# Kernel optimization log

Hardware: AMD Instinct MI355X
Metric: run time of the kernel (lower is better)

The kernel has to match this reference:

```python
import jax, jax.numpy as jnp
import numpy as np

NUM_ITERATIONS = 3


def _squash(s):
    # s: [B, J, S]. Faithful to the torch code: squash norm is computed over
    # dim=2 of s_j [B,1,J,S,1], i.e. the num_unit (J) axis here.
    mag_sq = jnp.sum(s * s, axis=1, keepdims=True)  # [B, 1, S]
    mag = jnp.sqrt(mag_sq)
    return s * (mag_sq / (1.0 + mag_sq) / mag)


def setup_inputs() -> dict:
    key = jax.random.key(0)
    k1, k2 = jax.random.split(key)
    B, U, C, J, S = 128, 8, 2048, 32, 16
    x = jax.random.normal(k1, (B, U, C), dtype=jnp.float32)
    W = jax.random.normal(k2, (1, C, J, S, U), dtype=jnp.float32)
    return {"x": x, "W": W}


def reference(x, W):
    # x: [B, in_unit, in_channel]; W: [1, C, J, S, U]
    xt = jnp.swapaxes(x, 1, 2)          # [B, C, U]
    Wc = W[0]                           # [C, J, S, U]
    # u_hat = W @ x (per input capsule c, output capsule j): [B, C, J, S]
    u_hat = jnp.einsum('cjsu,bcu->bcjs', Wc, xt)
    B, C, J, _ = u_hat.shape
    b = jnp.zeros((C, J), dtype=u_hat.dtype)
    v = None
    for _ in range(NUM_ITERATIONS):
        # legacy F.softmax on 4D [1,C,J,1] defaults to dim=1 -> over C
        c = jax.nn.softmax(b, axis=0)                      # [C, J]
        s = jnp.einsum('cj,bcjs->bjs', c, u_hat)           # [B, J, S]
        v = _squash(s)                                     # [B, J, S]
        # agreement, mean over batch (keepdim handled by shape [C,J])
        b = b + jnp.einsum('bcjs,bjs->cj', u_hat, v) / B
    return v[..., None]  # [B, num_unit, unit_size, 1] == v_j.squeeze(1)
```

## Files before the change

### kernel.cpp

```cpp
#include <hip/hip_runtime.h>
#include <hip/hip_bf16.h>

#define BB 128
#define UU 8
#define CC 2048
#define JJ 32
#define SS 16

typedef unsigned int u32;
typedef unsigned short u16;
typedef __attribute__((ext_vector_type(8))) short bf16x8;
typedef __attribute__((ext_vector_type(4))) float f32x4;

__device__ __forceinline__ float bflo(u32 p) { return __uint_as_float(p << 16); }
__device__ __forceinline__ float bfhi(u32 p) { return __uint_as_float(p & 0xffff0000u); }
__device__ __forceinline__ u32 f2b(float f) {
    u32 bits = __float_as_uint(f);
    u32 r = bits + 0x7fffu + ((bits >> 16) & 1u);
    return r >> 16;
}
__device__ __forceinline__ u32 pack2(float a, float b) { return f2b(a) | (f2b(b) << 16); }
__device__ __forceinline__ uint4 scale4(uint4 p, float cw) {
    uint4 o;
    o.x = pack2(bflo(p.x) * cw, bfhi(p.x) * cw);
    o.y = pack2(bflo(p.y) * cw, bfhi(p.y) * cw);
    o.z = pack2(bflo(p.z) * cw, bfhi(p.z) * cw);
    o.w = pack2(bflo(p.w) * cw, bfhi(p.w) * cw);
    return o;
}

__global__ __launch_bounds__(256) void k_prep(const float* __restrict__ x,
                                              const float* __restrict__ W,
                                              u16* __restrict__ xA,
                                              u16* __restrict__ xB,
                                              u16* __restrict__ Wn,
                                              float* __restrict__ bbp) {
    __shared__ uint4 ldsu[16][129];
    int blk = blockIdx.x, t = threadIdx.x;
    if (blk < 1024) {
        int b = blk >> 3;
        int c = (blk & 7) * 256 + t;
        const float* xf = x + (size_t)b * UU * CC;
        float v[8];
#pragma unroll
        for (int u = 0; u < 8; ++u) v[u] = xf[u * CC + c];
        uint4 p;
        p.x = pack2(v[0], v[1]);
        p.y = pack2(v[2], v[3]);
        p.z = pack2(v[4], v[5]);
        p.w = pack2(v[6], v[7]);
        ((uint4*)xA)[(size_t)b * CC + c] = p;
    } else if (blk < 2048) {
        int bb2 = blk - 1024;
        int u = bb2 >> 7, c0 = (bb2 & 127) * 16;
        float* ldsf = (float*)ldsu;
        int b = t >> 1, h = t & 1;
        const float4* x4 = (const float4*)(x + ((size_t)b * UU + u) * CC + c0);
        float4 lo = x4[h * 2], hi = x4[h * 2 + 1];
        ldsf[(h * 8 + 0) * 129 + b] = lo.x; ldsf[(h * 8 + 1) * 129 + b] = lo.y;
        ldsf[(h * 8 + 2) * 129 + b] = lo.z; ldsf[(h * 8 + 3) * 129 + b] = lo.w;
        ldsf[(h * 8 + 4) * 129 + b] = hi.x; ldsf[(h * 8 + 5) * 129 + b] = hi.y;
        ldsf[(h * 8 + 6) * 129 + b] = hi.z; ldsf[(h * 8 + 7) * 129 + b] = hi.w;
        __syncthreads();
        int ci = t >> 4, k8 = t & 15;
        const float* r = ldsf + ci * 129 + k8 * 8;
        uint4 p;
        p.x = pack2(r[0], r[1]);
        p.y = pack2(r[2], r[3]);
        p.z = pack2(r[4], r[5]);
        p.w = pack2(r[6], r[7]);
        ((uint4*)xB)[((size_t)u * CC + c0 + ci) * 16 + k8] = p;
    } else if (blk < 2560) {
        int bb2 = blk - 2048;
        int ct = bb2 & 127, nt = bb2 >> 7;
        int c0 = ct * 16, n0 = nt * 128;
        const float4* Wf = (const float4*)W;
        for (int q = t; q < 2048; q += 256) {
            int ci = q >> 7, ni = q & 127;
            size_t widx = (size_t)(c0 + ci) * 512 + n0 + ni;
            float4 lo = Wf[2 * widx], hi = Wf[2 * widx + 1];
            uint4 o;
            o.x = pack2(lo.x, lo.y);
            o.y = pack2(lo.z, lo.w);
            o.z = pack2(hi.x, hi.y);
            o.w = pack2(hi.z, hi.w);
            ldsu[ci][ni] = o;
        }
        __syncthreads();
        for (int q = t; q < 2048; q += 256) {
            int ni = q >> 4, ci = q & 15;
            ((uint4*)Wn)[(size_t)(n0 + ni) * 2048 + c0 + ci] = ldsu[ci][ni];
        }
    } else {
        int base = (blk - 2560) * 4096 + t;
#pragma unroll
        for (int r = 0; r < 16; ++r) bbp[base + r * 256] = 0.f;
    }
}

__global__ __launch_bounds__(256) void k_softmax(const float* __restrict__ bbp,
                                                 float* __restrict__ ccp) {
    int j = blockIdx.x, t = threadIdx.x;
    __shared__ float red[4];
    __shared__ float bcast[2];
    const float* row = bbp + j * CC;
    float m = -1e30f;
    for (int c = t; c < CC; c += 256) m = fmaxf(m, row[c]);
#pragma unroll
    for (int o = 32; o > 0; o >>= 1) m = fmaxf(m, __shfl_down(m, o, 64));
    if ((t & 63) == 0) red[t >> 6] = m;
    __syncthreads();
    if (t == 0) bcast[0] = fmaxf(fmaxf(red[0], red[1]), fmaxf(red[2], red[3]));
    __syncthreads();
    float mm = bcast[0];
    float ssum = 0.f;
    for (int c = t; c < CC; c += 256) ssum += expf(row[c] - mm);
#pragma unroll
    for (int o = 32; o > 0; o >>= 1) ssum += __shfl_down(ssum, o, 64);
    if ((t & 63) == 0) red[t >> 6] = ssum;
    __syncthreads();
    if (t == 0) bcast[1] = red[0] + red[1] + red[2] + red[3];
    __syncthreads();
    float inv = 1.0f / bcast[1];
    for (int c = t; c < CC; c += 256) ccp[j * CC + c] = expf(row[c] - mm) * inv;
}

__global__ __launch_bounds__(512) void k_gemmA(const u16* __restrict__ xA,
                                               const u16* __restrict__ Wn,
                                               const float* __restrict__ ccp,
                                               int use_cc,
                                               float* __restrict__ spart) {
    __shared__ uint4 As[128][9];
    __shared__ uint4 Bs[128][9];
    const uint4* xA4 = (const uint4*)xA;
    const uint4* Wn4 = (const uint4*)Wn;
    int t = threadIdx.x;
    int sl = blockIdx.x >> 2;
    int n0 = (blockIdx.x & 3) * 128;
    int w = t >> 6, lane = t & 63;
    int mh = w & 1, nq = w >> 1;
    int ln = lane & 15, quad = lane >> 4;
    f32x4 acc[4][2];
#pragma unroll
    for (int mt = 0; mt < 4; ++mt)
#pragma unroll
        for (int nt2 = 0; nt2 < 2; ++nt2) acc[mt][nt2] = {0.f, 0.f, 0.f, 0.f};

    for (int ch = 0; ch < 4; ++ch) {
        int cbase = sl * 32 + ch * 8;
#pragma unroll
        for (int r2 = 0; r2 < 2; ++r2) {
            int q = t + r2 * 512;
            int row = q >> 3, k8 = q & 7;
            As[row][k8] = xA4[(size_t)row * 2048 + cbase + k8];
        }
#pragma unroll
        for (int r2 = 0; r2 < 2; ++r2) {
            int q = t + r2 * 512;
            int ni = q >> 3, k8 = q & 7;
            uint4 wb = Wn4[(size_t)(n0 + ni) * 2048 + cbase + k8];
            if (use_cc) wb = scale4(wb, ccp[((n0 + ni) >> 4) * CC + cbase + k8]);
            Bs[ni][k8] = wb;
        }
        __syncthreads();
#pragma unroll
        for (int st = 0; st < 2; ++st) {
            bf16x8 af[4], bf[2];
#pragma unroll
            for (int mt = 0; mt < 4; ++mt)
                af[mt] = __builtin_bit_cast(bf16x8,
                         As[mh * 64 + mt * 16 + ln][st * 4 + quad]);
#pragma unroll
            for (int nt2 = 0; nt2 < 2; ++nt2)
                bf[nt2] = __builtin_bit_cast(bf16x8,
                          Bs[nq * 32 + nt2 * 16 + ln][st * 4 + quad]);
#pragma unroll
            for (int mt = 0; mt < 4; ++mt)
#pragma unroll
                for (int nt2 = 0; nt2 < 2; ++nt2)
                    acc[mt][nt2] = __builtin_amdgcn_mfma_f32_16x16x32_bf16(
                        af[mt], bf[nt2], acc[mt][nt2], 0, 0, 0);
        }
        __syncthreads();
    }
    float* outp = spart + sl * (BB * JJ * SS);
#pragma unroll
    for (int mt = 0; mt < 4; ++mt)
#pragma unroll
        for (int nt2 = 0; nt2 < 2; ++nt2)
#pragma unroll
            for (int r = 0; r < 4; ++r) {
                int b = mh * 64 + mt * 16 + quad * 4 + r;
                int n = n0 + nq * 32 + nt2 * 16 + ln;
                outp[b * 512 + n] = acc[mt][nt2][r];
            }
}

__global__ __launch_bounds__(512) void k_rsq(const float* __restrict__ spart,
                                             u16* __restrict__ vB,
                                             float* __restrict__ out,
                                             float scale_pre, int write_out) {
    __shared__ float s[512];
    __shared__ float sc[16];
    int b = blockIdx.x, n = threadIdx.x;
    float v = 0.f;
#pragma unroll
    for (int sl = 0; sl < 64; ++sl) v += spart[sl * (BB * JJ * SS) + b * 512 + n];
    v *= scale_pre;
    s[n] = v;
    __syncthreads();
    if (n < 16) {
        float msq = 0.f;
#pragma unroll
        for (int jj = 0; jj < 32; ++jj) {
            float tv = s[jj * 16 + n];
            msq = fmaf(tv, tv, msq);
        }
        sc[n] = msq / ((1.f + msq) * sqrtf(fmaxf(msq, 1e-30f)));
    }
    __syncthreads();
    float vv = s[n] * sc[n & 15];
    vB[n * BB + b] = (u16)f2b(vv);
    if (write_out) out[b * 512 + n] = vv;
}

__global__ __launch_bounds__(256) void k_gemmBf(const u16* __restrict__ vB,
                                                const u16* __restrict__ xB,
                                                const u16* __restrict__ Wn,
                                                float* __restrict__ bbp) {
    const bf16x8* A8 = (const bf16x8*)vB;
    const bf16x8* B8 = (const bf16x8*)xB;
    const uint4* Wn4 = (const uint4*)Wn;
    int t = threadIdx.x;
    int w = t >> 6, lane = t & 63;
    int gw = blockIdx.x * 4 + w;
    int u = gw >> 10, rest = gw & 1023;
    int nt = rest & 15, c0 = (rest >> 4) * 32;
    int n0 = nt * 32;
    int ln = lane & 15, quad = lane >> 4;
    bf16x8 av[2][4], bx[2][4];
#pragma unroll
    for (int mt = 0; mt < 2; ++mt)
#pragma unroll
        for (int st = 0; st < 4; ++st)
            av[mt][st] = A8[(n0 + mt * 16 + ln) * 16 + quad + 4 * st];
#pragma unroll
    for (int ct = 0; ct < 2; ++ct)
#pragma unroll
        for (int st = 0; st < 4; ++st)
            bx[ct][st] = B8[((size_t)u * CC + c0 + ct * 16 + ln) * 16 + quad + 4 * st];
    f32x4 acc[2][2];
    acc[0][0] = {0.f, 0.f, 0.f, 0.f};
    acc[0][1] = acc[0][0]; acc[1][0] = acc[0][0]; acc[1][1] = acc[0][0];
#pragma unroll
    for (int st = 0; st < 4; ++st)
#pragma unroll
        for (int mt = 0; mt < 2; ++mt)
#pragma unroll
            for (int ct = 0; ct < 2; ++ct)
                acc[mt][ct] = __builtin_amdgcn_mfma_f32_16x16x32_bf16(
                    av[mt][st], bx[ct][st], acc[mt][ct], 0, 0, 0);
#pragma unroll
    for (int mt = 0; mt < 2; ++mt) {
        int j = 2 * nt + mt;
#pragma unroll
        for (int ct = 0; ct < 2; ++ct) {
            int c = c0 + ct * 16 + ln;
            float val = 0.f;
#pragma unroll
            for (int r = 0; r < 4; ++r) {
                int n = n0 + mt * 16 + quad * 4 + r;
                uint4 wp = Wn4[(size_t)n * 2048 + c];
                u32 warr[4] = {wp.x, wp.y, wp.z, wp.w};
                u32 ww = warr[u >> 1];
                float wv = (u & 1) ? bfhi(ww) : bflo(ww);
                val = fmaf(acc[mt][ct][r], wv, val);
            }
            val += __shfl_xor(val, 16, 64);
            val += __shfl_xor(val, 32, 64);
            if (quad == 0)
                atomicAdd(&bbp[j * CC + c], val * (1.0f / BB));
        }
    }
}

extern "C" void kernel_launch(void* const* d_in, const int* in_sizes, int n_in,
                              void* d_out, int out_size, void* d_ws, size_t ws_size,
                              hipStream_t stream) {
    const float* x = (const float*)d_in[0];
    const float* W = (const float*)d_in[1];
    if (in_sizes[0] == CC * JJ * SS * UU) {
        x = (const float*)d_in[1];
        W = (const float*)d_in[0];
    }
    float* out = (float*)d_out;

    char* ws = (char*)d_ws;
    float* spart = (float*)ws;
    u16* xA = (u16*)(ws + (16u << 20));
    u16* xB = (u16*)(ws + (20u << 20));
    u16* Wn = (u16*)(ws + (24u << 20));
    size_t b48 = (size_t)48u << 20;
    u16* vB = (u16*)(ws + b48);
    float* bbp = (float*)(ws + b48 + 131072);
    float* ccp = (float*)(ws + b48 + 393216);

    k_prep<<<2576, 256, 0, stream>>>(x, W, xA, xB, Wn, bbp);

    for (int it = 0; it < 3; ++it) {
        if (it > 0) k_softmax<<<32, 256, 0, stream>>>(bbp, ccp);
        k_gemmA<<<256, 512, 0, stream>>>(xA, Wn, ccp, it > 0 ? 1 : 0, spart);
        k_rsq<<<128, 512, 0, stream>>>(spart, vB, out,
                                       it == 0 ? (1.0f / 2048.0f) : 1.0f,
                                       it == 2 ? 1 : 0);
        if (it < 2) k_gemmBf<<<2048, 256, 0, stream>>>(vB, xB, Wn, bbp);
    }
}
```

Before: 235.7 us.

## Drop LDS staging in gemmA, load MFMA fragments directly and split K further

The s-accumulation GEMM no longer stages A and B tiles through shared memory with barriers. Each wavefront now loads its bf16 fragments straight from global memory and computes a 64x64 output tile over a 64-channel K-slice, giving 128 K-slices instead of 64. This removes LDS traffic and synchronisation and adds parallelism. In exchange, the spart partial buffer doubles, the reduction in k_rsq reads twice as many slices, and the workspace layout is shifted to fit.

```diff
diff --git a/kernel.cpp b/kernel.cpp
--- a/kernel.cpp
+++ b/kernel.cpp
@@ -125,74 +125,65 @@
     for (int c = t; c < CC; c += 256) ccp[j * CC + c] = expf(row[c] - mm) * inv;
 }
 
-__global__ __launch_bounds__(512) void k_gemmA(const u16* __restrict__ xA,
+__global__ __launch_bounds__(256) void k_gemmA(const u16* __restrict__ xA,
                                                const u16* __restrict__ Wn,
                                                const float* __restrict__ ccp,
                                                int use_cc,
                                                float* __restrict__ spart) {
-    __shared__ uint4 As[128][9];
-    __shared__ uint4 Bs[128][9];
-    const uint4* xA4 = (const uint4*)xA;
-    const uint4* Wn4 = (const uint4*)Wn;
+    const bf16x8* A8 = (const bf16x8*)xA;
+    const uint4* B4 = (const uint4*)Wn;
     int t = threadIdx.x;
-    int sl = blockIdx.x >> 2;
-    int n0 = (blockIdx.x & 3) * 128;
     int w = t >> 6, lane = t & 63;
-    int mh = w & 1, nq = w >> 1;
+    int gw = blockIdx.x * 4 + w;
+    int sl = gw >> 4;
+    int rest = gw & 15;
+    int mg = rest & 1, ng = rest >> 1;
     int ln = lane & 15, quad = lane >> 4;
-    f32x4 acc[4][2];
+    int rowA[4], rowB[4];
+    const float* ccb[4];
+#pragma unroll
+    for (int mt = 0; mt < 4; ++mt) rowA[mt] = (mg * 64 + mt * 16 + ln) * 2048;
+#pragma unroll
+    for (int nt = 0; nt < 4; ++nt) {
+        rowB[nt] = (ng * 64 + nt * 16 + ln) * 2048;
+        ccb[nt] = ccp + (ng * 4 + nt) * CC;
+    }
+    int kk = sl * 16 + quad;
+    f32x4 acc[4][4];
 #pragma unroll
     for (int mt = 0; mt < 4; ++mt)
 #pragma unroll
-        for (int nt2 = 0; nt2 < 2; ++nt2) acc[mt][nt2] = {0.f, 0.f, 0.f, 0.f};
-
-    for (int ch = 0; ch < 4; ++ch) {
-        int cbase = sl * 32 + ch * 8;
-#pragma unroll
-        for (int r2 = 0; r2 < 2; ++r2) {
-            int q = t + r2 * 512;
-            int row = q >> 3, k8 = q & 7;
-            As[row][k8] = xA4[(size_t)row * 2048 + cbase + k8];
-        }
-#pragma unroll
-        for (int r2 = 0; r2 < 2; ++r2) {
-            int q = t + r2 * 512;
-            int ni = q >> 3, k8 = q & 7;
-            uint4 wb = Wn4[(size_t)(n0 + ni) * 2048 + cbase + k8];
-            if (use_cc) wb = scale4(wb, ccp[((n0 + ni) >> 4) * CC + cbase + k8]);
-            Bs[ni][k8] = wb;
-        }
-        __syncthreads();
-#pragma unroll
-        for (int st = 0; st < 2; ++st) {
-            bf16x8 af[4], bf[2];
-#pragma unroll
-            for (int mt = 0; mt < 4; ++mt)
-                af[mt] = __builtin_bit_cast(bf16x8,
-                         As[mh * 64 + mt * 16 + ln][st * 4 + quad]);
-#pragma unroll
-            for (int nt2 = 0; nt2 < 2; ++nt2)
-                bf[nt2] = __builtin_bit_cast(bf16x8,
-                          Bs[nq * 32 + nt2 * 16 + ln][st * 4 + quad]);
-#pragma unroll
-            for (int mt = 0; mt < 4; ++mt)
-#pragma unroll
-                for (int nt2 = 0; nt2 < 2; ++nt2)
-                    acc[mt][nt2] = __builtin_amdgcn_mfma_f32_16x16x32_bf16(
-                        af[mt], bf[nt2], acc[mt][nt2], 0, 0, 0);
-        }
-        __syncthreads();
+        for (int nt = 0; nt < 4; ++nt) acc[mt][nt] = {0.f, 0.f, 0.f, 0.f};
+#pragma unroll
+    for (int step = 0; step < 4; ++step) {
+        bf16x8 a[4];
+        uint4 wb[4];
+#pragma unroll
+        for (int mt = 0; mt < 4; ++mt) a[mt] = A8[rowA[mt] + kk];
+#pragma unroll
+        for (int nt = 0; nt < 4; ++nt) wb[nt] = B4[rowB[nt] + kk];
+        if (use_cc) {
+#pragma unroll
+            for (int nt = 0; nt < 4; ++nt) wb[nt] = scale4(wb[nt], ccb[nt][kk]);
+        }
+        kk += 4;
+#pragma unroll
+        for (int mt = 0; mt < 4; ++mt)
+#pragma unroll
+            for (int nt = 0; nt < 4; ++nt)
+                acc[mt][nt] = __builtin_amdgcn_mfma_f32_16x16x32_bf16(
+                    a[mt], __builtin_bit_cast(bf16x8, wb[nt]), acc[mt][nt], 0, 0, 0);
     }
     float* outp = spart + sl * (BB * JJ * SS);
 #pragma unroll
     for (int mt = 0; mt < 4; ++mt)
 #pragma unroll
-        for (int nt2 = 0; nt2 < 2; ++nt2)
+        for (int nt = 0; nt < 4; ++nt)
 #pragma unroll
             for (int r = 0; r < 4; ++r) {
-                int b = mh * 64 + mt * 16 + quad * 4 + r;
-                int n = n0 + nq * 32 + nt2 * 16 + ln;
-                outp[b * 512 + n] = acc[mt][nt2][r];
+                int b = mg * 64 + mt * 16 + quad * 4 + r;
+                int n = ng * 64 + nt * 16 + ln;
+                outp[b * 512 + n] = acc[mt][nt][r];
             }
 }
 
@@ -204,8 +195,8 @@
     __shared__ float sc[16];
     int b = blockIdx.x, n = threadIdx.x;
     float v = 0.f;
-#pragma unroll
-    for (int sl = 0; sl < 64; ++sl) v += spart[sl * (BB * JJ * SS) + b * 512 + n];
+#pragma unroll 16
+    for (int sl = 0; sl < 128; ++sl) v += spart[sl * (BB * JJ * SS) + b * 512 + n];
     v *= scale_pre;
     s[n] = v;
     __syncthreads();
@@ -297,19 +288,19 @@
 
     char* ws = (char*)d_ws;
     float* spart = (float*)ws;
-    u16* xA = (u16*)(ws + (16u << 20));
-    u16* xB = (u16*)(ws + (20u << 20));
-    u16* Wn = (u16*)(ws + (24u << 20));
-    size_t b48 = (size_t)48u << 20;
-    u16* vB = (u16*)(ws + b48);
-    float* bbp = (float*)(ws + b48 + 131072);
-    float* ccp = (float*)(ws + b48 + 393216);
+    u16* xA = (u16*)(ws + (32u << 20));
+    u16* xB = (u16*)(ws + (36u << 20));
+    u16* Wn = (u16*)(ws + (40u << 20));
+    size_t b64 = (size_t)64u << 20;
+    u16* vB = (u16*)(ws + b64);
+    float* bbp = (float*)(ws + b64 + 131072);
+    float* ccp = (float*)(ws + b64 + 393216);
 
     k_prep<<<2576, 256, 0, stream>>>(x, W, xA, xB, Wn, bbp);
 
     for (int it = 0; it < 3; ++it) {
         if (it > 0) k_softmax<<<32, 256, 0, stream>>>(bbp, ccp);
-        k_gemmA<<<256, 512, 0, stream>>>(xA, Wn, ccp, it > 0 ? 1 : 0, spart);
+        k_gemmA<<<512, 256, 0, stream>>>(xA, Wn, ccp, it > 0 ? 1 : 0, spart);
         k_rsq<<<128, 512, 0, stream>>>(spart, vB, out,
                                        it == 0 ? (1.0f / 2048.0f) : 1.0f,
                                        it == 2 ? 1 : 0);
```

After: 210.2 us. 10.8% less time.
